# Kernel tuning notes

Hardware: AMD Instinct MI355X
Metric: run time of the kernel (lower is better)

## Reference

```python
import jax, jax.numpy as jnp
import numpy as np

EPS = 1e-12
N, C, B = 8, 2048, 2048


def setup_inputs() -> dict:
    key = jax.random.key(0)
    kx, kk, kq = jax.random.split(key, 3)
    # Xavier-uniform bound for [C,C] weight
    bound = float(np.sqrt(6.0 / (C + C)))
    X = jax.random.normal(kx, (N, C, B), dtype=jnp.float32)
    Wk = jax.random.uniform(kk, (C, C), minval=-bound, maxval=bound, dtype=jnp.float32)
    Wq = jax.random.uniform(kq, (C, C), minval=-bound, maxval=bound, dtype=jnp.float32)
    Wk0 = jnp.zeros((C, 1), dtype=jnp.float32)
    Wq0 = jnp.zeros((C, 1), dtype=jnp.float32)
    return {"X": X, "Wk": Wk, "Wq": Wq, "Wk0": Wk0, "Wq0": Wq0}


def reference(X, Wk, Wq, Wk0, Wq0):
    # X: [N,C,B]; Wk,Wq: [C,C]; Wk0,Wq0: [C,1] (broadcast over B)
    K = jnp.einsum('ij,njb->nib', Wk, X) + Wk0  # [N,C,B]
    Q = jnp.einsum('ij,njb->nib', Wq, X) + Wq0  # [N,C,B]
    DK2 = jnp.sum(K * K, axis=2)  # [N,C] squared row norms
    DQ2 = jnp.sum(Q * Q, axis=2)  # [N,C]
    DQK = jnp.sqrt(jnp.maximum(DQ2[:, :, None] * DK2[:, None, :], EPS))  # [N,C,C]
    Y = jnp.einsum('nib,njb->nij', Q, K) / DQK  # cosine-normalized scores [N,C,C]
    SM = jax.nn.softmax(Y, axis=1)  # softmax over query-channel axis
    # Z = (X^T @ SM)^T : Z[n,j,b] = sum_c X[n,c,b] * SM[n,c,j]
    Z = jnp.einsum('ncb,ncj->njb', X, SM)  # [N,C,B]
    return Z
```

## Files before the change

### kernel.cpp

```cpp
#include <hip/hip_runtime.h>
#include <hip/hip_bf16.h>

typedef __bf16 bf16_t;
typedef __bf16 bf16x8 __attribute__((ext_vector_type(8)));
typedef __bf16 bf16x4 __attribute__((ext_vector_type(4)));
typedef float  f32x4  __attribute__((ext_vector_type(4)));

#define NB 8
#define CD 2048
#define BD 2048
#define LD 2048
#define BK 64
#define NT (LD / BK)
#define NP (NT / 2)

#define BAR()     __builtin_amdgcn_s_barrier()
#define WAITL0()  asm volatile("s_waitcnt lgkmcnt(0)")
#define WAITL8()  asm volatile("s_waitcnt lgkmcnt(8)")
#define WAITV(n)  asm volatile("s_waitcnt vmcnt(" #n ")" ::: "memory")

__global__ void k_transpose_x(const float* __restrict__ X, bf16_t* __restrict__ XbT) {
    __shared__ bf16_t tile[64][66];
    const int t = threadIdx.x;
    const int b0 = blockIdx.x * 64, c0 = blockIdx.y * 64, n = blockIdx.z;
    const float* Xn = X + (size_t)n * CD * BD;
    bf16_t* Tn = XbT + (size_t)n * BD * CD;
    const int cl = t & 63, rw = t >> 6;
#pragma unroll
    for (int r = 0; r < 16; ++r) {
        int row = r * 4 + rw;
        tile[row][cl] = (bf16_t)Xn[(size_t)(c0 + row) * BD + b0 + cl];
    }
    __syncthreads();
#pragma unroll
    for (int r = 0; r < 16; ++r) {
        int row = r * 4 + rw;
        Tn[(size_t)(b0 + row) * CD + c0 + cl] = tile[cl][row];
    }
}

__global__ void k_convert_w(const float* __restrict__ Wk, const float* __restrict__ Wq,
                            bf16_t* __restrict__ Wkb, bf16_t* __restrict__ Wqb) {
    const size_t i = ((size_t)blockIdx.x * 256 + threadIdx.x) * 4;
    const float* src = blockIdx.y ? Wq : Wk;
    bf16_t* dst = blockIdx.y ? Wqb : Wkb;
    float4 v = *(const float4*)(src + i);
    bf16x4 o;
    o[0] = (bf16_t)v.x; o[1] = (bf16_t)v.y; o[2] = (bf16_t)v.z; o[3] = (bf16_t)v.w;
    *(bf16x4*)(dst + i) = o;
}


__device__ __forceinline__ void gll16(const bf16_t* g, bf16_t* l) {
    __builtin_amdgcn_global_load_lds((const __attribute__((address_space(1))) void*)g,
                                     (__attribute__((address_space(3))) void*)l, 16, 0, 0);
}

__device__ __forceinline__ void stage_half(const bf16_t* gsrc, bf16_t* ldsh, int w, int l) {
    const int rr = l >> 3;
    const int ce = ((l & 7) ^ rr) * 8;
#pragma unroll
    for (int i = 0; i < 2; ++i) {
        const bf16_t* g = gsrc + (size_t)(i * 64 + w * 8 + rr) * LD + ce;
        gll16(g, ldsh + i * 4096 + w * 512);
    }
}

__device__ __forceinline__ bf16x8 lds_frag(const bf16_t* hbase, int row16, int lr, int st, int ks, int swz) {
    const int r = row16 + lr;
    const int ce = (st * 32 + ks * 8) ^ swz;
    return *(const bf16x8*)(hbase + r * 64 + ce);
}

template <int EPI>
__global__ __launch_bounds__(512, 2) void k_gemm256(const bf16_t* __restrict__ Aall, size_t sA,
                                                    const bf16_t* __restrict__ Ball, size_t sB,
                                                    void* __restrict__ Call, size_t sC,
                                                    const float* __restrict__ bias) {
    __shared__ alignas(16) bf16_t As[2][2][128 * 64];
    __shared__ alignas(16) bf16_t Bs[2][2][128 * 64];
    const int tid = threadIdx.x;
    const int lane = tid & 63, wave = tid >> 6;
    const int wm = wave >> 2, wn = wave & 3;
    const int lr = lane & 15, ks = lane >> 4;
    const int swz = (lr & 7) << 3;

    const int bid = blockIdx.x;
    const int lin = (bid & 7) * 64 + (bid >> 3);
    const int z = lin >> 6, rem = lin & 63, bm = rem >> 3, bn = rem & 7;
    const int m0 = bm * 256, n0 = bn * 256;

    const bf16_t* Ab = Aall + sA * z + (size_t)m0 * LD;
    const bf16_t* Bb = Ball + sB * z + (size_t)n0 * LD;

    stage_half(Ab,                 &As[0][0][0], wave, lane);
    stage_half(Bb,                 &Bs[0][0][0], wave, lane);
    stage_half(Ab + 128 * LD,      &As[0][1][0], wave, lane);
    stage_half(Bb + 128 * LD,      &Bs[0][1][0], wave, lane);
    WAITV(4);
    stage_half(Ab + BK,            &As[1][0][0], wave, lane);
    stage_half(Bb + BK,            &Bs[1][0][0], wave, lane);
    stage_half(Bb + 128 * LD + BK, &Bs[1][1][0], wave, lane);
    WAITV(6);
    BAR();

    f32x4 acc[2][2][4][2] = {};
    bf16x8 afr[4][2], bf0[2][2], bf1[2][2];

    auto RD_A = [&](int slot, int half) {
#pragma unroll
        for (int mi = 0; mi < 4; ++mi)
#pragma unroll
            for (int st = 0; st < 2; ++st)
                afr[mi][st] = lds_frag(&As[slot][half][0], wm * 64 + mi * 16, lr, st, ks, swz);
    };
    auto RD_B = [&](bf16x8 (&dst)[2][2], int slot, int half) {
#pragma unroll
        for (int ni = 0; ni < 2; ++ni)
#pragma unroll
            for (int st = 0; st < 2; ++st)
                dst[ni][st] = lds_frag(&Bs[slot][half][0], wn * 32 + ni * 16, lr, st, ks, swz);
    };
    auto MFMA_Q = [&](int mh, int nh, bf16x8 (&bsrc)[2][2]) {
        __builtin_amdgcn_s_setprio(1);
#pragma unroll
        for (int st = 0; st < 2; ++st)
#pragma unroll
            for (int mi = 0; mi < 4; ++mi)
#pragma unroll
                for (int ni = 0; ni < 2; ++ni)
                    acc[mh][nh][mi][ni] = __builtin_amdgcn_mfma_f32_16x16x32_bf16(
                        afr[mi][st], bsrc[ni][st], acc[mh][nh][mi][ni], 0, 0, 0);
        __builtin_amdgcn_s_setprio(0);
    };

    for (int tp = 0; tp < NP; ++tp) {
        const int u = 2 * tp, v = u + 1;
        const int w = (u + 2 < NT) ? u + 2 : NT - 1;
        const int x = (v + 2 < NT) ? v + 2 : NT - 1;

        RD_A(0, 0); RD_B(bf0, 0, 0);
        stage_half(Ab + 128 * LD + v * BK, &As[1][1][0], wave, lane);
        WAITL8();
        BAR(); WAITL0();
        MFMA_Q(0, 0, bf0);
        BAR();

        RD_B(bf1, 0, 1);
        stage_half(Ab + w * BK, &As[0][0][0], wave, lane);
        BAR(); WAITL0();
        MFMA_Q(0, 1, bf1);
        BAR();

        RD_A(0, 1);
        stage_half(Bb + w * BK, &Bs[0][0][0], wave, lane);
        BAR(); WAITL0();
        MFMA_Q(1, 0, bf0);
        BAR();

        stage_half(Bb + 128 * LD + w * BK, &Bs[0][1][0], wave, lane);
        WAITV(6);
        BAR();
        MFMA_Q(1, 1, bf1);
        BAR();

        RD_A(1, 0); RD_B(bf0, 1, 0);
        stage_half(Ab + 128 * LD + w * BK, &As[0][1][0], wave, lane);
        WAITL8();
        BAR(); WAITL0();
        MFMA_Q(0, 0, bf0);
        BAR();

        RD_B(bf1, 1, 1);
        stage_half(Ab + x * BK, &As[1][0][0], wave, lane);
        BAR(); WAITL0();
        MFMA_Q(0, 1, bf1);
        BAR();

        RD_A(1, 1);
        stage_half(Bb + x * BK, &Bs[1][0][0], wave, lane);
        BAR(); WAITL0();
        MFMA_Q(1, 0, bf0);
        BAR();

        stage_half(Bb + 128 * LD + x * BK, &Bs[1][1][0], wave, lane);
        WAITV(6);
        BAR();
        MFMA_Q(1, 1, bf1);
        BAR();
    }
    WAITV(0);

    const int rsub = ks * 4;
#pragma unroll
    for (int mh = 0; mh < 2; ++mh)
#pragma unroll
        for (int mi = 0; mi < 4; ++mi)
#pragma unroll
            for (int j = 0; j < 4; ++j) {
                const int r = m0 + mh * 128 + wm * 64 + mi * 16 + rsub + j;
                float bv = 0.f;
                if (EPI == 1) bv = bias[r];
#pragma unroll
                for (int nh = 0; nh < 2; ++nh)
#pragma unroll
                    for (int ni = 0; ni < 2; ++ni) {
                        const int c = n0 + nh * 128 + wn * 32 + ni * 16 + lr;
                        const float vv = acc[mh][nh][mi][ni][j] + bv;
                        if (EPI == 0) ((float*)Call)[sC * z + (size_t)r * LD + c] = vv;
                        else          ((bf16_t*)Call)[sC * z + (size_t)r * LD + c] = (bf16_t)vv;
                    }
            }
}

__global__ void k_row_norm2(const bf16_t* __restrict__ Kb, const bf16_t* __restrict__ Qb,
                            float* __restrict__ DK2, float* __restrict__ DQ2) {
    const int row = blockIdx.x, n = blockIdx.y;
    const bf16_t* src = blockIdx.z ? Qb : Kb;
    float* dst = blockIdx.z ? DQ2 : DK2;
    const bf16_t* pr = src + ((size_t)n * CD + row) * BD + threadIdx.x * 8;
    bf16x8 v = *(const bf16x8*)pr;
    float s = 0.f;
#pragma unroll
    for (int e = 0; e < 8; ++e) { float x = (float)v[e]; s += x * x; }
#pragma unroll
    for (int off = 32; off; off >>= 1) s += __shfl_xor(s, off, 64);
    __shared__ float ws[4];
    if ((threadIdx.x & 63) == 0) ws[threadIdx.x >> 6] = s;
    __syncthreads();
    if (threadIdx.x == 0) dst[(size_t)n * CD + row] = ws[0] + ws[1] + ws[2] + ws[3];
}

__global__ void k_softmax_rows(const bf16_t* __restrict__ Yt, const float* __restrict__ DK2,
                               const float* __restrict__ DQ2, bf16_t* __restrict__ SMT) {
    const int j = blockIdx.x, n = blockIdx.y, t = threadIdx.x;
    const int lane = t & 63, wave = t >> 6;
    const bf16_t* y = Yt + ((size_t)n * CD + j) * CD;
    const float* q2 = DQ2 + (size_t)n * CD;
    const float dk2 = DK2[(size_t)n * CD + j];
    const int i0 = t * 8;

    bf16x8 yr = *(const bf16x8*)(y + i0);
    float4 qa = *(const float4*)(q2 + i0);
    float4 qb = *(const float4*)(q2 + i0 + 4);
    float qv[8] = {qa.x, qa.y, qa.z, qa.w, qb.x, qb.y, qb.z, qb.w};
    float v[8];
#pragma unroll
    for (int e = 0; e < 8; ++e)
        v[e] = (float)yr[e] * rsqrtf(fmaxf(dk2 * qv[e], 1e-12f));

    float m = v[0];
#pragma unroll
    for (int e = 1; e < 8; ++e) m = fmaxf(m, v[e]);
#pragma unroll
    for (int off = 32; off; off >>= 1) m = fmaxf(m, __shfl_xor(m, off, 64));
    __shared__ float redm[4], reds[4];
    if (lane == 0) redm[wave] = m;
    __syncthreads();
    m = fmaxf(fmaxf(redm[0], redm[1]), fmaxf(redm[2], redm[3]));

    float e8[8];
    float s = 0.f;
#pragma unroll
    for (int e = 0; e < 8; ++e) { e8[e] = __expf(v[e] - m); s += e8[e]; }
#pragma unroll
    for (int off = 32; off; off >>= 1) s += __shfl_xor(s, off, 64);
    if (lane == 0) reds[wave] = s;
    __syncthreads();
    s = reds[0] + reds[1] + reds[2] + reds[3];
    const float inv = 1.f / s;

    bf16x8 o;
#pragma unroll
    for (int e = 0; e < 8; ++e) o[e] = (bf16_t)(e8[e] * inv);
    *(bf16x8*)(SMT + ((size_t)n * CD + j) * CD + i0) = o;
}

extern "C" void kernel_launch(void* const* d_in, const int* in_sizes, int n_in,
                              void* d_out, int out_size, void* d_ws, size_t ws_size,
                              hipStream_t stream) {
    const float* X   = (const float*)d_in[0];
    const float* Wk  = (const float*)d_in[1];
    const float* Wq  = (const float*)d_in[2];
    const float* Wk0 = (const float*)d_in[3];
    const float* Wq0 = (const float*)d_in[4];
    float* Z = (float*)d_out;

    const size_t NCB = (size_t)NB * CD * BD;
    const size_t CC  = (size_t)CD * CD;
    const size_t NCC = (size_t)NB * CC;

    char* p = (char*)d_ws;
    bf16_t* XbT = (bf16_t*)p; p += NCB * 2;
    bf16_t* Wkb = (bf16_t*)p; p += CC * 2;
    bf16_t* Wqb = (bf16_t*)p; p += CC * 2;
    bf16_t* Kb  = (bf16_t*)p; p += NCB * 2;
    bf16_t* Qb  = (bf16_t*)p; p += NCB * 2;
    float*  DK2 = (float*)p;  p += (size_t)NB * CD * 4;
    float*  DQ2 = (float*)p;  p += (size_t)NB * CD * 4;
    bf16_t* Yt  = (bf16_t*)p; p += NCC * 2;
    bf16_t* SMT = Kb;
    if ((size_t)(p - (char*)d_ws) > ws_size) return;

    dim3 blk(256);
    k_transpose_x<<<dim3(BD / 64, CD / 64, NB), blk, 0, stream>>>(X, XbT);
    k_convert_w<<<dim3(CC / 1024, 2), blk, 0, stream>>>(Wk, Wq, Wkb, Wqb);
    k_gemm256<1><<<512, 512, 0, stream>>>(Wkb, 0, XbT, (size_t)BD * CD, Kb, (size_t)CD * BD, Wk0);
    k_gemm256<1><<<512, 512, 0, stream>>>(Wqb, 0, XbT, (size_t)BD * CD, Qb, (size_t)CD * BD, Wq0);
    k_row_norm2<<<dim3(CD, NB, 2), blk, 0, stream>>>(Kb, Qb, DK2, DQ2);
    k_gemm256<2><<<512, 512, 0, stream>>>(Kb, (size_t)CD * BD, Qb, (size_t)CD * BD, Yt, CC, nullptr);
    k_softmax_rows<<<dim3(CD, NB), blk, 0, stream>>>(Yt, DK2, DQ2, SMT);
    k_gemm256<0><<<512, 512, 0, stream>>>(SMT, CC, XbT, (size_t)BD * CD, Z, (size_t)CD * BD, nullptr);
}
```

Before: 578.5 us.

## Prefetch LDS fragments one phase ahead with double-buffered A registers

Adds a second A-fragment register set so LDS fragment reads for the next MFMA quadrant are issued before the current quadrant's MFMAs, and removes the explicit lgkmcnt waits. The aim is to hide LDS read latency behind matrix-core work instead of stalling at each phase. This raises register pressure, and the waits are now left to the compiler, which may place them conservatively or expose ordering hazards with the global-to-LDS staging.

```diff
diff --git a/kernel.cpp b/kernel.cpp
--- a/kernel.cpp
+++ b/kernel.cpp
@@ -15,8 +15,6 @@
 #define NP (NT / 2)
 
 #define BAR()     __builtin_amdgcn_s_barrier()
-#define WAITL0()  asm volatile("s_waitcnt lgkmcnt(0)")
-#define WAITL8()  asm volatile("s_waitcnt lgkmcnt(8)")
 #define WAITV(n)  asm volatile("s_waitcnt vmcnt(" #n ")" ::: "memory")
 
 __global__ void k_transpose_x(const float* __restrict__ X, bf16_t* __restrict__ XbT) {
@@ -105,14 +103,14 @@
     BAR();
 
     f32x4 acc[2][2][4][2] = {};
-    bf16x8 afr[4][2], bf0[2][2], bf1[2][2];
-
-    auto RD_A = [&](int slot, int half) {
+    bf16x8 afrE[4][2], afrO[4][2], bf0[2][2], bf1[2][2];
+
+    auto RD_A = [&](bf16x8 (&dst)[4][2], int slot, int half) {
 #pragma unroll
         for (int mi = 0; mi < 4; ++mi)
 #pragma unroll
             for (int st = 0; st < 2; ++st)
-                afr[mi][st] = lds_frag(&As[slot][half][0], wm * 64 + mi * 16, lr, st, ks, swz);
+                dst[mi][st] = lds_frag(&As[slot][half][0], wm * 64 + mi * 16, lr, st, ks, swz);
     };
     auto RD_B = [&](bf16x8 (&dst)[2][2], int slot, int half) {
 #pragma unroll
@@ -121,7 +119,7 @@
             for (int st = 0; st < 2; ++st)
                 dst[ni][st] = lds_frag(&Bs[slot][half][0], wn * 32 + ni * 16, lr, st, ks, swz);
     };
-    auto MFMA_Q = [&](int mh, int nh, bf16x8 (&bsrc)[2][2]) {
+    auto MFMA_Q = [&](int mh, int nh, bf16x8 (&asrc)[4][2], bf16x8 (&bsrc)[2][2]) {
         __builtin_amdgcn_s_setprio(1);
 #pragma unroll
         for (int st = 0; st < 2; ++st)
@@ -130,63 +128,63 @@
 #pragma unroll
                 for (int ni = 0; ni < 2; ++ni)
                     acc[mh][nh][mi][ni] = __builtin_amdgcn_mfma_f32_16x16x32_bf16(
-                        afr[mi][st], bsrc[ni][st], acc[mh][nh][mi][ni], 0, 0, 0);
+                        asrc[mi][st], bsrc[ni][st], acc[mh][nh][mi][ni], 0, 0, 0);
         __builtin_amdgcn_s_setprio(0);
     };
+
+    RD_A(afrE, 0, 0); RD_B(bf0, 0, 0);
 
     for (int tp = 0; tp < NP; ++tp) {
         const int u = 2 * tp, v = u + 1;
         const int w = (u + 2 < NT) ? u + 2 : NT - 1;
         const int x = (v + 2 < NT) ? v + 2 : NT - 1;
 
-        RD_A(0, 0); RD_B(bf0, 0, 0);
+        RD_B(bf1, 0, 1);
         stage_half(Ab + 128 * LD + v * BK, &As[1][1][0], wave, lane);
-        WAITL8();
-        BAR(); WAITL0();
-        MFMA_Q(0, 0, bf0);
-        BAR();
-
-        RD_B(bf1, 0, 1);
+        BAR();
+        MFMA_Q(0, 0, afrE, bf0);
+        BAR();
+
+        RD_A(afrO, 0, 1);
         stage_half(Ab + w * BK, &As[0][0][0], wave, lane);
-        BAR(); WAITL0();
-        MFMA_Q(0, 1, bf1);
-        BAR();
-
-        RD_A(0, 1);
+        BAR();
+        MFMA_Q(0, 1, afrE, bf1);
+        BAR();
+
         stage_half(Bb + w * BK, &Bs[0][0][0], wave, lane);
-        BAR(); WAITL0();
-        MFMA_Q(1, 0, bf0);
+        BAR();
+        MFMA_Q(1, 0, afrO, bf0);
         BAR();
 
         stage_half(Bb + 128 * LD + w * BK, &Bs[0][1][0], wave, lane);
         WAITV(6);
         BAR();
-        MFMA_Q(1, 1, bf1);
-        BAR();
-
-        RD_A(1, 0); RD_B(bf0, 1, 0);
+        RD_A(afrE, 1, 0); RD_B(bf0, 1, 0);
+        MFMA_Q(1, 1, afrO, bf1);
+        BAR();
+
+        RD_B(bf1, 1, 1);
         stage_half(Ab + 128 * LD + w * BK, &As[0][1][0], wave, lane);
-        WAITL8();
-        BAR(); WAITL0();
-        MFMA_Q(0, 0, bf0);
-        BAR();
-
-        RD_B(bf1, 1, 1);
+        BAR();
+        MFMA_Q(0, 0, afrE, bf0);
+        BAR();
+
+        RD_A(afrO, 1, 1);
         stage_half(Ab + x * BK, &As[1][0][0], wave, lane);
-        BAR(); WAITL0();
-        MFMA_Q(0, 1, bf1);
-        BAR();
-
-        RD_A(1, 1);
+        BAR();
+        MFMA_Q(0, 1, afrE, bf1);
+        BAR();
+
         stage_half(Bb + x * BK, &Bs[1][0][0], wave, lane);
-        BAR(); WAITL0();
-        MFMA_Q(1, 0, bf0);
+        BAR();
+        MFMA_Q(1, 0, afrO, bf0);
         BAR();
 
         stage_half(Bb + 128 * LD + x * BK, &Bs[1][1][0], wave, lane);
         WAITV(6);
         BAR();
-        MFMA_Q(1, 1, bf1);
+        RD_A(afrE, 0, 0); RD_B(bf0, 0, 0);
+        MFMA_Q(1, 1, afrO, bf1);
         BAR();
     }
     WAITV(0);
```

New measurement: 577.6 us. Within noise of the previous version (-0.2%).
